# Performance work log

Hardware: AMD Instinct MI355X
Metric: run time of the kernel (lower is better)

## Reference

```python
import jax, jax.numpy as jnp
import numpy as np

B, T, U, D = 2, 512, 48, 512
H, K = 1024, 128  # hidden_channels, num_classes; fc1 in = 2*D = 1024


def setup_inputs() -> dict:
    key = jax.random.key(0)
    ks = jax.random.split(key, 9)
    s = 0.02
    return {
        "img_feature": jax.random.normal(ks[0], (B, T, D), jnp.float32),
        "label_feature": jax.random.normal(ks[1], (B, U, D), jnp.float32),
        "masks": jnp.ones((B, 1, T), jnp.float32),
        "W1": jax.random.normal(ks[2], (H, 2 * D), jnp.float32) * s,
        "b1": jnp.zeros((H,), jnp.float32),
        "W2": jax.random.normal(ks[3], (K, H), jnp.float32) * s,
        "b2": jnp.zeros((K,), jnp.float32),
        "conv_w": jax.random.normal(ks[4], (K, D), jnp.float32) * s,
        "conv_b": jnp.zeros((K,), jnp.float32),
    }


def reference(img_feature, label_feature, masks, W1, b1, W2, b2, conv_w, conv_b):
    # pointwise Conv1d over img features: (B,T,D) -> (B,K,T), masked
    img_seg_score = (jnp.einsum('btd,kd->bkt', img_feature, conv_w)
                     + conv_b[None, :, None]) * masks
    # fc1(cat(label, img)) == label @ Wl^T + img @ Wi^T + b1 (broadcast add),
    # avoiding the O(B*U*T*2D) repeat+cat intermediate.
    d = label_feature.shape[-1]
    Wl, Wi = W1[:, :d], W1[:, d:]
    lab = jnp.einsum('bud,hd->buh', label_feature, Wl)  # (B,U,H)
    img = jnp.einsum('btd,hd->bth', img_feature, Wi)    # (B,T,H)
    h = jnp.tanh(lab[:, :, None, :] + img[:, None, :, :] + b1)  # (B,U,T,H)
    joint = jnp.einsum('buth,kh->butk', h, W2) + b2
    joint_score = jax.nn.log_softmax(joint, axis=-1)
    return (img_seg_score, joint_score)
```

## Files before the change

kernel.cpp:

```cpp
#include <hip/hip_runtime.h>
#include <math.h>

#define BB 2
#define TT 512
#define UU 48
#define DD 512
#define HH 1024
#define KK 128

typedef _Float16 f16x8 __attribute__((ext_vector_type(8)));
typedef __fp16 fp16x2_t __attribute__((ext_vector_type(2)));
typedef float floatx4 __attribute__((ext_vector_type(4)));

__device__ __forceinline__ f16x8 tanh8(f16x8 x) {
    f16x8 o;
#pragma unroll
    for (int i = 0; i < 8; i += 2) {
        float s0 = (float)x[i];
        float s1 = (float)x[i + 1];
        float e0 = __expf(s0 + s0);
        float e1 = __expf(s1 + s1);
        float r0 = __builtin_amdgcn_rcpf(e0 + 1.0f);
        float r1 = __builtin_amdgcn_rcpf(e1 + 1.0f);
        fp16x2_t p = __builtin_amdgcn_cvt_pkrtz(fmaf(-2.0f, r0, 1.0f),
                                                fmaf(-2.0f, r1, 1.0f));
        o[i] = (_Float16)p[0];
        o[i + 1] = (_Float16)p[1];
    }
    return o;
}

__global__ __launch_bounds__(256) void mid_kernel4(
    const float* __restrict__ img, const float* __restrict__ labf,
    const float* __restrict__ W1, const float* __restrict__ W2,
    const float* __restrict__ conv_w,
    const float* __restrict__ b1, const float* __restrict__ conv_b,
    const float* __restrict__ masks,
    _Float16* __restrict__ imgHf, _Float16* __restrict__ labHf,
    _Float16* __restrict__ W2s, float* __restrict__ seg_out) {
    int bid = blockIdx.x, tid = threadIdx.x;
    if (bid >= 312) {
        int base = (bid - 312) * 256 + tid;
#pragma unroll
        for (int i = 0; i < 32; ++i) {
            int o = base + i * 4096;
            int hg = o >> 10, kk2 = (o >> 3) & 127, hl = o & 7;
            W2s[o] = (_Float16)W2[(size_t)kk2 * HH + hg * 8 + hl];
        }
        return;
    }
    __shared__ __align__(16) _Float16 a_s[32][72];
    __shared__ __align__(16) _Float16 w_s[8192];
    const float* Arow;
    const float* Wbase;
    int r0, n0b, wstride, region;
    if (bid < 256) {
        region = 0; Arow = img; Wbase = W1 + 512; wstride = 1024;
        r0 = (bid & 31) * 32; n0b = (bid >> 5) * 128;
    } else if (bid < 280) {
        region = 1; Arow = labf; Wbase = W1; wstride = 1024;
        int i = bid - 256; r0 = (i % 3) * 32; n0b = (i / 3) * 128;
    } else {
        region = 2; Arow = img; Wbase = conv_w; wstride = 512;
        r0 = (bid - 280) * 32; n0b = 0;
    }
    int lane = tid & 63, wv = tid >> 6;
    int m0 = (wv & 1) * 16, n0w = (wv >> 1) * 64;
    int q = lane >> 4, r = lane & 15;
    int arow = tid >> 3, acol = (tid & 7) * 8;
    int wn = tid >> 3, wk = tid & 7;
    const float* aptr = &Arow[(size_t)(r0 + arow) * DD + acol];
    floatx4 acc[4] = {};
    float4 pa0, pa1, pw[4][2];
    pa0 = *(const float4*)aptr;
    pa1 = *(const float4*)(aptr + 4);
#pragma unroll
    for (int i2 = 0; i2 < 4; ++i2) {
        const float* wp_ = &Wbase[(size_t)(n0b + i2 * 32 + wn) * wstride + wk * 8];
        pw[i2][0] = *(const float4*)wp_;
        pw[i2][1] = *(const float4*)(wp_ + 4);
    }
    for (int c = 0; c < 8; ++c) {
        {
            f16x8 av;
            av[0] = (_Float16)pa0.x; av[1] = (_Float16)pa0.y;
            av[2] = (_Float16)pa0.z; av[3] = (_Float16)pa0.w;
            av[4] = (_Float16)pa1.x; av[5] = (_Float16)pa1.y;
            av[6] = (_Float16)pa1.z; av[7] = (_Float16)pa1.w;
            *(f16x8*)&a_s[arow][acol] = av;
#pragma unroll
            for (int i2 = 0; i2 < 4; ++i2) {
                f16x8 wvv;
                wvv[0] = (_Float16)pw[i2][0].x; wvv[1] = (_Float16)pw[i2][0].y;
                wvv[2] = (_Float16)pw[i2][0].z; wvv[3] = (_Float16)pw[i2][0].w;
                wvv[4] = (_Float16)pw[i2][1].x; wvv[5] = (_Float16)pw[i2][1].y;
                wvv[6] = (_Float16)pw[i2][1].z; wvv[7] = (_Float16)pw[i2][1].w;
                *(f16x8*)&w_s[((size_t)wk * 128 + i2 * 32 + wn) * 8] = wvv;
            }
        }
        __syncthreads();
        if (c < 7) {
            int cb = (c + 1) * 64;
            pa0 = *(const float4*)(aptr + cb);
            pa1 = *(const float4*)(aptr + cb + 4);
#pragma unroll
            for (int i2 = 0; i2 < 4; ++i2) {
                const float* wp_ =
                    &Wbase[(size_t)(n0b + i2 * 32 + wn) * wstride + cb + wk * 8];
                pw[i2][0] = *(const float4*)wp_;
                pw[i2][1] = *(const float4*)(wp_ + 4);
            }
        }
#pragma unroll
        for (int kt = 0; kt < 2; ++kt) {
            f16x8 af = *(const f16x8*)&a_s[m0 + r][kt * 32 + q * 8];
#pragma unroll
            for (int nt = 0; nt < 4; ++nt) {
                f16x8 bfv = *(const f16x8*)
                    &w_s[((kt * 4 + q) * 128 + n0w + nt * 16 + r) * 8];
                acc[nt] = __builtin_amdgcn_mfma_f32_16x16x32_f16(
                    af, bfv, acc[nt], 0, 0, 0);
            }
        }
        __syncthreads();
    }
    if (region == 0) {
#pragma unroll
        for (int nt = 0; nt < 4; ++nt) {
            int n = n0b + n0w + nt * 16 + r;
#pragma unroll
            for (int rr = 0; rr < 4; ++rr)
                imgHf[(size_t)(r0 + m0 + 4 * q + rr) * HH + n] =
                    (_Float16)acc[nt][rr];
        }
    } else if (region == 1) {
#pragma unroll
        for (int nt = 0; nt < 4; ++nt) {
            int n = n0b + n0w + nt * 16 + r;
            float bv = b1[n];
#pragma unroll
            for (int rr = 0; rr < 4; ++rr)
                labHf[(size_t)(r0 + m0 + 4 * q + rr) * HH + n] =
                    (_Float16)(acc[nt][rr] + bv);
        }
    } else {
#pragma unroll
        for (int nt = 0; nt < 4; ++nt) {
            int k = n0w + nt * 16 + r;
            float bv = conv_b[k];
#pragma unroll
            for (int rr = 0; rr < 4; ++rr) {
                int row = r0 + m0 + 4 * q + rr;
                int b = row >> 9, t = row & 511;
                seg_out[((size_t)b * KK + k) * TT + t] =
                    (acc[nt][rr] + bv) * masks[row];
            }
        }
    }
}

__global__ __launch_bounds__(256) void joint_kernel6(
    const _Float16* __restrict__ imgHf,
    const _Float16* __restrict__ labHf,
    const _Float16* __restrict__ W2s,
    const float* __restrict__ b2,
    float* __restrict__ out) {
    __shared__ __align__(16) _Float16 w_s[2][8192];
    int tid = threadIdx.x, bid = blockIdx.x;
    int t0 = (bid & 7) * 64;
    int rest = bid >> 3;
    int u = rest % UU, b = rest / UU;
    int lane = tid & 63, wv = tid >> 6;
    int q = lane >> 4, r = lane & 15;
    const _Float16* imgrow = imgHf + ((size_t)b * TT + t0 + wv * 16 + r) * HH;
    const _Float16* labrow = labHf + (size_t)(b * UU + u) * HH;
    int c0 = q * 8, c1 = 32 + q * 8;
    int ws_off = tid * 8;
    floatx4 acc[8] = {};
    f16x8 ivA = *(const f16x8*)&imgrow[c0];
    f16x8 ivB = *(const f16x8*)&imgrow[c1];
    f16x8 lvA = *(const f16x8*)&labrow[c0];
    f16x8 lvB = *(const f16x8*)&labrow[c1];
    {
        const _Float16* wsrc = W2s;
#pragma unroll
        for (int i2 = 0; i2 < 4; ++i2)
            *(f16x8*)&w_s[0][i2 * 2048 + ws_off] =
                *(const f16x8*)&wsrc[i2 * 2048 + ws_off];
    }
    __syncthreads();
#pragma unroll 2
    for (int c = 0; c < 16; ++c) {
        int buf = c & 1;
        f16x8 nivA, nivB, nlvA, nlvB, nw0, nw1, nw2, nw3;
        if (c < 15) {
            int cb = (c + 1) * 64;
            nivA = *(const f16x8*)&imgrow[cb + c0];
            nivB = *(const f16x8*)&imgrow[cb + c1];
            nlvA = *(const f16x8*)&labrow[cb + c0];
            nlvB = *(const f16x8*)&labrow[cb + c1];
            const _Float16* wsrc = W2s + (size_t)(c + 1) * 8192;
            nw0 = *(const f16x8*)&wsrc[0 * 2048 + ws_off];
            nw1 = *(const f16x8*)&wsrc[1 * 2048 + ws_off];
            nw2 = *(const f16x8*)&wsrc[2 * 2048 + ws_off];
            nw3 = *(const f16x8*)&wsrc[3 * 2048 + ws_off];
        }
        f16x8 a0 = tanh8(ivA + lvA);
        f16x8 a1 = tanh8(ivB + lvB);
#pragma unroll
        for (int nt = 0; nt < 8; ++nt) {
            f16x8 bf0 = *(const f16x8*)&w_s[buf][((0 + q) * 128 + nt * 16 + r) * 8];
            acc[nt] = __builtin_amdgcn_mfma_f32_16x16x32_f16(
                a0, bf0, acc[nt], 0, 0, 0);
        }
#pragma unroll
        for (int nt = 0; nt < 8; ++nt) {
            f16x8 bf1 = *(const f16x8*)&w_s[buf][((4 + q) * 128 + nt * 16 + r) * 8];
            acc[nt] = __builtin_amdgcn_mfma_f32_16x16x32_f16(
                a1, bf1, acc[nt], 0, 0, 0);
        }
        if (c < 15) {
            *(f16x8*)&w_s[buf ^ 1][0 * 2048 + ws_off] = nw0;
            *(f16x8*)&w_s[buf ^ 1][1 * 2048 + ws_off] = nw1;
            *(f16x8*)&w_s[buf ^ 1][2 * 2048 + ws_off] = nw2;
            *(f16x8*)&w_s[buf ^ 1][3 * 2048 + ws_off] = nw3;
            ivA = nivA; ivB = nivB; lvA = nlvA; lvB = nlvB;
        }
        __syncthreads();
    }
    float b2v[8];
#pragma unroll
    for (int nt = 0; nt < 8; ++nt) b2v[nt] = b2[nt * 16 + r];
    float* orow = out + (((size_t)b * UU + u) * TT + t0 + wv * 16) * KK;
#pragma unroll
    for (int rr = 0; rr < 4; ++rr) {
        float v[8];
        float mx = -INFINITY;
#pragma unroll
        for (int nt = 0; nt < 8; ++nt) {
            v[nt] = acc[nt][rr] + b2v[nt];
            mx = fmaxf(mx, v[nt]);
        }
        mx = fmaxf(mx, __shfl_xor(mx, 1, 16));
        mx = fmaxf(mx, __shfl_xor(mx, 2, 16));
        mx = fmaxf(mx, __shfl_xor(mx, 4, 16));
        mx = fmaxf(mx, __shfl_xor(mx, 8, 16));
        float s = 0.f;
#pragma unroll
        for (int nt = 0; nt < 8; ++nt) s += __expf(v[nt] - mx);
        s += __shfl_xor(s, 1, 16);
        s += __shfl_xor(s, 2, 16);
        s += __shfl_xor(s, 4, 16);
        s += __shfl_xor(s, 8, 16);
        float lse = mx + __logf(s);
        int row = 4 * q + rr;
#pragma unroll
        for (int nt = 0; nt < 8; ++nt)
            orow[(size_t)row * KK + nt * 16 + r] = v[nt] - lse;
    }
}

extern "C" void kernel_launch(void* const* d_in, const int* in_sizes, int n_in,
                              void* d_out, int out_size, void* d_ws, size_t ws_size,
                              hipStream_t stream) {
    const float* img    = (const float*)d_in[0];
    const float* labf   = (const float*)d_in[1];
    const float* masks  = (const float*)d_in[2];
    const float* W1     = (const float*)d_in[3];
    const float* b1     = (const float*)d_in[4];
    const float* W2     = (const float*)d_in[5];
    const float* b2     = (const float*)d_in[6];
    const float* conv_w = (const float*)d_in[7];
    const float* conv_b = (const float*)d_in[8];
    float* out = (float*)d_out;

    _Float16* base  = (_Float16*)d_ws;
    _Float16* imgHf = base;
    _Float16* labHf = imgHf + 1024 * 1024;
    _Float16* W2s   = labHf + 96 * 1024;

    mid_kernel4<<<328, 256, 0, stream>>>(img, labf, W1, W2, conv_w,
                                         b1, conv_b, masks,
                                         imgHf, labHf, W2s, out);
    joint_kernel6<<<768, 256, 0, stream>>>(imgHf, labHf, W2s, b2,
                                           out + (size_t)BB * KK * TT);
}
```

Before: 123.6 us.

## Enlarge img projection tiles to 64x128 per block to halve grid size

The img and conv projection blocks in the first kernel now compute 64-row by 128-column tiles, with each wave handling 16 rows across all 128 columns (8 accumulators), instead of 32-row tiles. This halves the number of blocks and the redundant reloading and conversion of W1/conv_w slices per row tile. The label projection keeps its old 32-row path in a separate branch. The trade-off is more registers per thread and fewer blocks (184 vs 328) on a GPU with many CUs, which may leave CUs idle. The joint kernel, which likely dominates total time, is unchanged.

```diff
diff --git a/kernel.cpp b/kernel.cpp
--- a/kernel.cpp
+++ b/kernel.cpp
@@ -30,7 +30,16 @@
     return o;
 }
 
-__global__ __launch_bounds__(256) void mid_kernel4(
+__device__ __forceinline__ f16x8 cvt8(float4 a, float4 b) {
+    f16x8 v;
+    v[0] = (_Float16)a.x; v[1] = (_Float16)a.y;
+    v[2] = (_Float16)a.z; v[3] = (_Float16)a.w;
+    v[4] = (_Float16)b.x; v[5] = (_Float16)b.y;
+    v[6] = (_Float16)b.z; v[7] = (_Float16)b.w;
+    return v;
+}
+
+__global__ __launch_bounds__(256) void mid_kernel5(
     const float* __restrict__ img, const float* __restrict__ labf,
     const float* __restrict__ W1, const float* __restrict__ W2,
     const float* __restrict__ conv_w,
@@ -39,8 +48,8 @@
     _Float16* __restrict__ imgHf, _Float16* __restrict__ labHf,
     _Float16* __restrict__ W2s, float* __restrict__ seg_out) {
     int bid = blockIdx.x, tid = threadIdx.x;
-    if (bid >= 312) {
-        int base = (bid - 312) * 256 + tid;
+    if (bid >= 168) {
+        int base = (bid - 168) * 256 + tid;
 #pragma unroll
         for (int i = 0; i < 32; ++i) {
             int o = base + i * 4096;
@@ -49,31 +58,89 @@
         }
         return;
     }
-    __shared__ __align__(16) _Float16 a_s[32][72];
+    __shared__ __align__(16) _Float16 a_s[64][72];
     __shared__ __align__(16) _Float16 w_s[8192];
-    const float* Arow;
-    const float* Wbase;
-    int r0, n0b, wstride, region;
-    if (bid < 256) {
-        region = 0; Arow = img; Wbase = W1 + 512; wstride = 1024;
-        r0 = (bid & 31) * 32; n0b = (bid >> 5) * 128;
-    } else if (bid < 280) {
-        region = 1; Arow = labf; Wbase = W1; wstride = 1024;
-        int i = bid - 256; r0 = (i % 3) * 32; n0b = (i / 3) * 128;
-    } else {
-        region = 2; Arow = img; Wbase = conv_w; wstride = 512;
-        r0 = (bid - 280) * 32; n0b = 0;
-    }
     int lane = tid & 63, wv = tid >> 6;
-    int m0 = (wv & 1) * 16, n0w = (wv >> 1) * 64;
     int q = lane >> 4, r = lane & 15;
     int arow = tid >> 3, acol = (tid & 7) * 8;
     int wn = tid >> 3, wk = tid & 7;
-    const float* aptr = &Arow[(size_t)(r0 + arow) * DD + acol];
-    floatx4 acc[4] = {};
-    float4 pa0, pa1, pw[4][2];
-    pa0 = *(const float4*)aptr;
-    pa1 = *(const float4*)(aptr + 4);
+
+    if (bid >= 128 && bid < 152) {
+        int i = bid - 128;
+        int r0 = (i % 3) * 32, n0b = (i / 3) * 128;
+        int m0 = (wv & 1) * 16, n0w = (wv >> 1) * 64;
+        const float* aptr = &labf[(size_t)(r0 + (arow & 31)) * DD + acol];
+        floatx4 acc[4] = {};
+        float4 pa0, pa1, pw[4][2];
+        pa0 = *(const float4*)aptr;
+        pa1 = *(const float4*)(aptr + 4);
+#pragma unroll
+        for (int i2 = 0; i2 < 4; ++i2) {
+            const float* wp_ = &W1[(size_t)(n0b + i2 * 32 + wn) * 1024 + wk * 8];
+            pw[i2][0] = *(const float4*)wp_;
+            pw[i2][1] = *(const float4*)(wp_ + 4);
+        }
+        for (int c = 0; c < 8; ++c) {
+            *(f16x8*)&a_s[arow & 31][acol] = cvt8(pa0, pa1);
+#pragma unroll
+            for (int i2 = 0; i2 < 4; ++i2)
+                *(f16x8*)&w_s[((size_t)wk * 128 + i2 * 32 + wn) * 8] =
+                    cvt8(pw[i2][0], pw[i2][1]);
+            __syncthreads();
+            if (c < 7) {
+                int cb = (c + 1) * 64;
+                pa0 = *(const float4*)(aptr + cb);
+                pa1 = *(const float4*)(aptr + cb + 4);
+#pragma unroll
+                for (int i2 = 0; i2 < 4; ++i2) {
+                    const float* wp_ =
+                        &W1[(size_t)(n0b + i2 * 32 + wn) * 1024 + cb + wk * 8];
+                    pw[i2][0] = *(const float4*)wp_;
+                    pw[i2][1] = *(const float4*)(wp_ + 4);
+                }
+            }
+#pragma unroll
+            for (int kt = 0; kt < 2; ++kt) {
+                f16x8 af = *(const f16x8*)&a_s[m0 + r][kt * 32 + q * 8];
+#pragma unroll
+                for (int nt = 0; nt < 4; ++nt) {
+                    f16x8 bfv = *(const f16x8*)
+                        &w_s[((kt * 4 + q) * 128 + n0w + nt * 16 + r) * 8];
+                    acc[nt] = __builtin_amdgcn_mfma_f32_16x16x32_f16(
+                        af, bfv, acc[nt], 0, 0, 0);
+                }
+            }
+            __syncthreads();
+        }
+#pragma unroll
+        for (int nt = 0; nt < 4; ++nt) {
+            int n = n0b + n0w + nt * 16 + r;
+            float bv = b1[n];
+#pragma unroll
+            for (int rr = 0; rr < 4; ++rr)
+                labHf[(size_t)(r0 + m0 + 4 * q + rr) * HH + n] =
+                    (_Float16)(acc[nt][rr] + bv);
+        }
+        return;
+    }
+
+    const float* Wbase;
+    int r0, n0b, wstride, region;
+    if (bid < 128) {
+        region = 0; Wbase = W1 + 512; wstride = 1024;
+        r0 = (bid & 15) * 64; n0b = (bid >> 4) * 128;
+    } else {
+        region = 2; Wbase = conv_w; wstride = 512;
+        r0 = (bid - 152) * 64; n0b = 0;
+    }
+    const float* aptr0 = &img[(size_t)(r0 + arow) * DD + acol];
+    const float* aptr1 = aptr0 + (size_t)32 * DD;
+    floatx4 acc[8] = {};
+    float4 pa[4], pw[4][2];
+    pa[0] = *(const float4*)aptr0;
+    pa[1] = *(const float4*)(aptr0 + 4);
+    pa[2] = *(const float4*)aptr1;
+    pa[3] = *(const float4*)(aptr1 + 4);
 #pragma unroll
     for (int i2 = 0; i2 < 4; ++i2) {
         const float* wp_ = &Wbase[(size_t)(n0b + i2 * 32 + wn) * wstride + wk * 8];
@@ -81,28 +148,19 @@
         pw[i2][1] = *(const float4*)(wp_ + 4);
     }
     for (int c = 0; c < 8; ++c) {
-        {
-            f16x8 av;
-            av[0] = (_Float16)pa0.x; av[1] = (_Float16)pa0.y;
-            av[2] = (_Float16)pa0.z; av[3] = (_Float16)pa0.w;
-            av[4] = (_Float16)pa1.x; av[5] = (_Float16)pa1.y;
-            av[6] = (_Float16)pa1.z; av[7] = (_Float16)pa1.w;
-            *(f16x8*)&a_s[arow][acol] = av;
-#pragma unroll
-            for (int i2 = 0; i2 < 4; ++i2) {
-                f16x8 wvv;
-                wvv[0] = (_Float16)pw[i2][0].x; wvv[1] = (_Float16)pw[i2][0].y;
-                wvv[2] = (_Float16)pw[i2][0].z; wvv[3] = (_Float16)pw[i2][0].w;
-                wvv[4] = (_Float16)pw[i2][1].x; wvv[5] = (_Float16)pw[i2][1].y;
-                wvv[6] = (_Float16)pw[i2][1].z; wvv[7] = (_Float16)pw[i2][1].w;
-                *(f16x8*)&w_s[((size_t)wk * 128 + i2 * 32 + wn) * 8] = wvv;
-            }
-        }
+        *(f16x8*)&a_s[arow][acol] = cvt8(pa[0], pa[1]);
+        *(f16x8*)&a_s[arow + 32][acol] = cvt8(pa[2], pa[3]);
+#pragma unroll
+        for (int i2 = 0; i2 < 4; ++i2)
+            *(f16x8*)&w_s[((size_t)wk * 128 + i2 * 32 + wn) * 8] =
+                cvt8(pw[i2][0], pw[i2][1]);
         __syncthreads();
         if (c < 7) {
             int cb = (c + 1) * 64;
-            pa0 = *(const float4*)(aptr + cb);
-            pa1 = *(const float4*)(aptr + cb + 4);
+            pa[0] = *(const float4*)(aptr0 + cb);
+            pa[1] = *(const float4*)(aptr0 + cb + 4);
+            pa[2] = *(const float4*)(aptr1 + cb);
+            pa[3] = *(const float4*)(aptr1 + cb + 4);
 #pragma unroll
             for (int i2 = 0; i2 < 4; ++i2) {
                 const float* wp_ =
@@ -113,11 +171,11 @@
         }
 #pragma unroll
         for (int kt = 0; kt < 2; ++kt) {
-            f16x8 af = *(const f16x8*)&a_s[m0 + r][kt * 32 + q * 8];
-#pragma unroll
-            for (int nt = 0; nt < 4; ++nt) {
+            f16x8 af = *(const f16x8*)&a_s[wv * 16 + r][kt * 32 + q * 8];
+#pragma unroll
+            for (int nt = 0; nt < 8; ++nt) {
                 f16x8 bfv = *(const f16x8*)
-                    &w_s[((kt * 4 + q) * 128 + n0w + nt * 16 + r) * 8];
+                    &w_s[((kt * 4 + q) * 128 + nt * 16 + r) * 8];
                 acc[nt] = __builtin_amdgcn_mfma_f32_16x16x32_f16(
                     af, bfv, acc[nt], 0, 0, 0);
             }
@@ -126,31 +184,21 @@
     }
     if (region == 0) {
 #pragma unroll
-        for (int nt = 0; nt < 4; ++nt) {
-            int n = n0b + n0w + nt * 16 + r;
+        for (int nt = 0; nt < 8; ++nt) {
+            int n = n0b + nt * 16 + r;
 #pragma unroll
             for (int rr = 0; rr < 4; ++rr)
-                imgHf[(size_t)(r0 + m0 + 4 * q + rr) * HH + n] =
+                imgHf[(size_t)(r0 + wv * 16 + 4 * q + rr) * HH + n] =
                     (_Float16)acc[nt][rr];
         }
-    } else if (region == 1) {
-#pragma unroll
-        for (int nt = 0; nt < 4; ++nt) {
-            int n = n0b + n0w + nt * 16 + r;
-            float bv = b1[n];
-#pragma unroll
-            for (int rr = 0; rr < 4; ++rr)
-                labHf[(size_t)(r0 + m0 + 4 * q + rr) * HH + n] =
-                    (_Float16)(acc[nt][rr] + bv);
-        }
     } else {
 #pragma unroll
-        for (int nt = 0; nt < 4; ++nt) {
-            int k = n0w + nt * 16 + r;
+        for (int nt = 0; nt < 8; ++nt) {
+            int k = nt * 16 + r;
             float bv = conv_b[k];
 #pragma unroll
             for (int rr = 0; rr < 4; ++rr) {
-                int row = r0 + m0 + 4 * q + rr;
+                int row = r0 + wv * 16 + 4 * q + rr;
                 int b = row >> 9, t = row & 511;
                 seg_out[((size_t)b * KK + k) * TT + t] =
                     (acc[nt][rr] + bv) * masks[row];
@@ -279,7 +327,7 @@
     _Float16* labHf = imgHf + 1024 * 1024;
     _Float16* W2s   = labHf + 96 * 1024;
 
-    mid_kernel4<<<328, 256, 0, stream>>>(img, labf, W1, W2, conv_w,
+    mid_kernel5<<<184, 256, 0, stream>>>(img, labf, W1, W2, conv_w,
                                          b1, conv_b, masks,
                                          imgHf, labHf, W2s, out);
     joint_kernel6<<<768, 256, 0, stream>>>(imgHf, labHf, W2s, b2,
```

Result: slower. 129.7 us (+5.0%).
